# Kernel optimization log

Hardware: AMD Instinct MI355X
Metric: run time of the kernel (lower is better)

Reference implementation:

```python
import jax, jax.numpy as jnp
import numpy as np

MODEL_DIM = 2048
NUM_HEADS = 32
NUM_KV_HEADS = 8
HEAD_DIM = MODEL_DIM // NUM_HEADS  # 64
NUM_REP = NUM_HEADS // NUM_KV_HEADS  # 4


def setup_inputs() -> dict:
    key = jax.random.key(0)
    ks = jax.random.split(key, 6)
    B, S = 1, 2048
    s = 1.0 / np.sqrt(MODEL_DIM)
    x = jax.random.normal(ks[0], (B, S, MODEL_DIM), dtype=jnp.float32)
    # causal mask, 1 = keep, 0 = mask (scores.masked_fill(mask == 0, -1e9))
    mask = jnp.tril(jnp.ones((S, S), dtype=jnp.int32))[None, None, :, :]
    w_q = jax.random.normal(ks[1], (MODEL_DIM, MODEL_DIM), dtype=jnp.float32) * s
    w_k = jax.random.normal(ks[2], (NUM_KV_HEADS * HEAD_DIM, MODEL_DIM), dtype=jnp.float32) * s
    w_v = jax.random.normal(ks[3], (NUM_KV_HEADS * HEAD_DIM, MODEL_DIM), dtype=jnp.float32) * s
    w_o = jax.random.normal(ks[4], (MODEL_DIM, MODEL_DIM), dtype=jnp.float32) * s
    b_o = jax.random.normal(ks[5], (MODEL_DIM,), dtype=jnp.float32) * 0.01
    return {"x": x, "mask": mask, "w_q": w_q, "w_k": w_k, "w_v": w_v, "w_o": w_o, "b_o": b_o}


def reference(x, mask, w_q, w_k, w_v, w_o, b_o):
    B, S, _ = x.shape
    # projections (torch Linear: x @ W.T)
    q = (x @ w_q.T).reshape(B, S, NUM_HEADS, HEAD_DIM).transpose(0, 2, 1, 3)      # [B,H,S,D]
    k = (x @ w_k.T).reshape(B, S, NUM_KV_HEADS, HEAD_DIM).transpose(0, 2, 1, 3)   # [B,Hk,S,D]
    v = (x @ w_v.T).reshape(B, S, NUM_KV_HEADS, HEAD_DIM).transpose(0, 2, 1, 3)   # [B,Hk,S,D]
    # group Q heads by their shared KV head instead of materializing repeated KV
    qg = q.reshape(B, NUM_KV_HEADS, NUM_REP, S, HEAD_DIM)                         # [B,Hk,R,S,D]
    scale = 1.0 / np.sqrt(HEAD_DIM).astype(np.float32)
    scores = jnp.einsum('bgrsd,bgtd->bgrst', qg, k) * scale                       # [B,Hk,R,S,S]
    scores = jnp.where(mask[:, :, None, :, :] == 0, jnp.float32(-1e9), scores)
    attn = jax.nn.softmax(scores, axis=-1)
    ctx = jnp.einsum('bgrst,bgtd->bgrsd', attn, v)                                # [B,Hk,R,S,D]
    ctx = ctx.reshape(B, NUM_HEADS, S, HEAD_DIM).transpose(0, 2, 1, 3).reshape(B, S, MODEL_DIM)
    return ctx @ w_o.T + b_o
```

## Files before the change

### kernel.cpp

```cpp
#include <hip/hip_runtime.h>
#include <hip/hip_bf16.h>

typedef __hip_bfloat16 bf16;
typedef __attribute__((ext_vector_type(8))) short short8;
typedef __attribute__((ext_vector_type(4))) short short4_t;
typedef __attribute__((ext_vector_type(4))) float f32x4;

#define S_LEN 2048
#define DMODEL 2048
#define NH 32
#define NKV 8
#define DH 64

__device__ __forceinline__ int detect_isbf(const void* src) {
    unsigned int wsamp = ((const unsigned int*)src)[(threadIdx.x & 63) * 37];
    int e0 = (wsamp >> 7) & 0xFF;
    unsigned long long mb = __ballot(e0 >= 100 && e0 <= 140);
    return (__popcll(mb) >= 48) ? 1 : 0;
}

__global__ void detect_kernel(const unsigned int* __restrict__ x, int* __restrict__ flag) {
    int tid = threadIdx.x;
    unsigned int w = x[tid * 37];
    int e0 = (w >> 7) & 0xFF;
    int in = (e0 >= 100 && e0 <= 140) ? 1 : 0;
    unsigned long long m = __ballot(in);
    if (tid == 0) flag[0] = (__popcll(m) >= 48) ? 1 : 0;
}

__device__ __forceinline__ void conv8(const void* src, bf16* dst, int i, float scale, int isbf) {
    short8 out;
    if (isbf) {
        short8 v = *(const short8*)((const bf16*)src + i);
        if (scale != 1.0f) {
            #pragma unroll
            for (int j = 0; j < 8; ++j) {
                float f = __bfloat162float(((const bf16*)&v)[j]) * scale;
                ((bf16*)&out)[j] = __float2bfloat16(f);
            }
        } else out = v;
    } else {
        const float* gp = (const float*)src + i;
        f32x4 a = *(const f32x4*)gp;
        f32x4 b = *(const f32x4*)(gp + 4);
        #pragma unroll
        for (int j = 0; j < 4; ++j) ((bf16*)&out)[j]     = __float2bfloat16(a[j] * scale);
        #pragma unroll
        for (int j = 0; j < 4; ++j) ((bf16*)&out)[j + 4] = __float2bfloat16(b[j] * scale);
    }
    *(short8*)(dst + i) = out;
}

__global__ __launch_bounds__(256)
void convert4_kernel(const void* __restrict__ x, const void* __restrict__ wq,
                     const void* __restrict__ wk, const void* __restrict__ wv,
                     bf16* __restrict__ xb, bf16* __restrict__ wqkv) {
    const int b = blockIdx.x;
    const void* src; bf16* dst; int boff; float scale = 1.0f;
    if (b < 2048)       { src = x;  dst = xb;              boff = b;        }
    else if (b < 4096)  { src = wq; dst = wqkv;            boff = b - 2048; scale = 0.125f; }
    else if (b < 4608)  { src = wk; dst = wqkv + 4194304;  boff = b - 4096; }
    else                { src = wv; dst = wqkv + 5242880;  boff = b - 4608; }
    const int isbf = detect_isbf(src);
    int i = (boff * 256 + threadIdx.x) * 8;
    conv8(src, dst, i, scale, isbf);
}

__device__ __forceinline__ void gload_lds16(const void* g, void* l) {
    __builtin_amdgcn_global_load_lds(
        (const __attribute__((address_space(1))) void*)(unsigned long long)(size_t)g,
        (__attribute__((address_space(3))) void*)(unsigned int)(size_t)l,
        16, 0, 0);
}

__device__ __forceinline__ void gemm_core_2ph(const bf16* __restrict__ A, const bf16* __restrict__ B,
                                              int K, int m0, int n0,
                                              bf16* sA, bf16* sB, f32x4 acc[4][2]) {
    const int tid = threadIdx.x;
    const int w = tid >> 6, lane = tid & 63;
    const int wm = (w >> 1) * 64, wn = (w & 1) * 32;
    const int lm = lane & 15, lq = lane >> 4;
    const int xr = lm & 7;

    size_t aoff[4], boff[2];
    #pragma unroll
    for (int r = 0; r < 4; ++r) {
        int ci = w * 256 + r * 64 + lane;
        int row = ci >> 3, c = (ci & 7) ^ (row & 7);
        aoff[r] = (size_t)(m0 + row) * K + c * 8;
    }
    #pragma unroll
    for (int r = 0; r < 2; ++r) {
        int cj = w * 128 + r * 64 + lane;
        int row = cj >> 3, c = (cj & 7) ^ (row & 7);
        boff[r] = (size_t)(n0 + row) * K + c * 8;
    }

    const int nt = K >> 6;
    int cur = 0;

    {
        bf16* la = sA + w * 2048;
        bf16* lb = sB + w * 1024;
        #pragma unroll
        for (int r = 0; r < 4; ++r) gload_lds16(A + aoff[r], la + r * 512);
        #pragma unroll
        for (int r = 0; r < 2; ++r) gload_lds16(B + boff[r], lb + r * 512);
    }
    __syncthreads();

    for (int t = 0; t < nt; ++t) {
        bf16* curA = sA + cur * 8192;
        bf16* curB = sB + cur * 4096;
        if (t + 1 < nt) {
            const int nxt = cur ^ 1;
            const int k0 = (t + 1) << 6;
            bf16* la = sA + nxt * 8192 + w * 2048;
            bf16* lb = sB + nxt * 4096 + w * 1024;
            #pragma unroll
            for (int r = 0; r < 4; ++r) gload_lds16(A + aoff[r] + k0, la + r * 512);
            #pragma unroll
            for (int r = 0; r < 2; ++r) gload_lds16(B + boff[r] + k0, lb + r * 512);
        }

        short8 aF[2][4], bF[2][2];
        #pragma unroll
        for (int ks = 0; ks < 2; ++ks) {
            const int cc = ((ks * 4 + lq) ^ xr) * 8;
            #pragma unroll
            for (int i = 0; i < 4; ++i)
                aF[ks][i] = *(const short8*)&curA[(wm + i * 16 + lm) * 64 + cc];
            #pragma unroll
            for (int j = 0; j < 2; ++j)
                bF[ks][j] = *(const short8*)&curB[(wn + j * 16 + lm) * 64 + cc];
        }

        __builtin_amdgcn_s_setprio(1);
        #pragma unroll
        for (int ks = 0; ks < 2; ++ks)
            #pragma unroll
            for (int i = 0; i < 4; ++i)
                #pragma unroll
                for (int j = 0; j < 2; ++j)
                    acc[i][j] = __builtin_amdgcn_mfma_f32_16x16x32_bf16(aF[ks][i], bF[ks][j], acc[i][j], 0, 0, 0);
        __builtin_amdgcn_s_setprio(0);

        __syncthreads();
        cur ^= 1;
    }
}

template<bool BIAS, bool BIAS_DYN, bool OUT_DYN>
__global__ __launch_bounds__(256, 3)
void gemm_bf16s(const bf16* __restrict__ A, const bf16* __restrict__ B,
                const void* __restrict__ bias, void* __restrict__ C,
                int M, int N, int K, int ldc, const void* __restrict__ xsrc) {
    __shared__ bf16 sA[2 * 128 * 64];
    __shared__ bf16 sB[2 * 64 * 64];
    const int isbf = (BIAS_DYN || OUT_DYN) ? detect_isbf(xsrc) : 1;
    const int tid = threadIdx.x;
    const int m0 = blockIdx.y * 128, n0 = blockIdx.x * 64;
    const int w = tid >> 6, lane = tid & 63;
    const int wm = (w >> 1) * 64, wn = (w & 1) * 32;
    const int lm = lane & 15, lq = lane >> 4;

    f32x4 acc[4][2];
    const f32x4 zero = {0.f, 0.f, 0.f, 0.f};
    for (int i = 0; i < 4; ++i)
        for (int j = 0; j < 2; ++j) acc[i][j] = zero;

    gemm_core_2ph(A, B, K, m0, n0, sA, sB, acc);

    for (int i = 0; i < 4; ++i)
        for (int j = 0; j < 2; ++j)
            for (int r = 0; r < 4; ++r) {
                int row = m0 + wm + i * 16 + lq * 4 + r;
                int col = n0 + wn + j * 16 + lm;
                float v = acc[i][j][r];
                if (BIAS) {
                    if (BIAS_DYN && !isbf) v += ((const float*)bias)[col];
                    else                   v += __bfloat162float(((const bf16*)bias)[col]);
                }
                size_t idx = (size_t)row * ldc + col;
                if (OUT_DYN && !isbf) ((float*)C)[idx] = v;
                else                  ((bf16*)C)[idx] = __float2bfloat16(v);
            }
}

__global__ __launch_bounds__(256, 3)
void gemm_qkv(const bf16* __restrict__ A, const bf16* __restrict__ B,
              bf16* __restrict__ Qo, bf16* __restrict__ Ko, bf16* __restrict__ Vto) {
    __shared__ bf16 sA[2 * 128 * 64];
    __shared__ bf16 sB[2 * 64 * 64];
    const int tid = threadIdx.x;
    const int m0 = blockIdx.y * 128, n0 = blockIdx.x * 64;
    const int w = tid >> 6, lane = tid & 63;
    const int wm = (w >> 1) * 64, wn = (w & 1) * 32;
    const int lm = lane & 15, lq = lane >> 4;

    f32x4 acc[4][2];
    const f32x4 zero = {0.f, 0.f, 0.f, 0.f};
    for (int i = 0; i < 4; ++i)
        for (int j = 0; j < 2; ++j) acc[i][j] = zero;

    gemm_core_2ph(A, B, DMODEL, m0, n0, sA, sB, acc);

    const int route = (n0 < 2048) ? 0 : ((n0 < 2560) ? 1 : 2);
    for (int i = 0; i < 4; ++i)
        for (int j = 0; j < 2; ++j)
            for (int r = 0; r < 4; ++r) {
                int row = m0 + wm + i * 16 + lq * 4 + r;
                int col = n0 + wn + j * 16 + lm;
                bf16 v = __float2bfloat16(acc[i][j][r]);
                if (route == 0)      Qo[(size_t)row * DMODEL + col] = v;
                else if (route == 1) Ko[(size_t)row * (NKV * DH) + (col - 2048)] = v;
                else                 Vto[(size_t)(col - 2560) * S_LEN + row] = v;
            }
}

template<bool TRANS_OUT, bool BIAS, bool A_DYN, bool B_DYN, bool BIAS_DYN, bool OUT_DYN>
__global__ __launch_bounds__(256, 2)
void gemm_bt(const void* __restrict__ A, const void* __restrict__ B,
             const void* __restrict__ bias, void* __restrict__ C,
             int M, int N, int K, int ldc, const int* __restrict__ flagp) {
    __shared__ bf16 sA[128 * 32];
    __shared__ bf16 sB[128 * 32];

    const int isbf = flagp[0];
    const int tid = threadIdx.x;
    const int m0 = blockIdx.y * 128, n0 = blockIdx.x * 128;
    const int w = tid >> 6, lane = tid & 63;
    const int wm = (w >> 1) * 64, wn = (w & 1) * 64;
    const int lm = lane & 15, lq = lane >> 4;

    f32x4 acc[4][4];
    const f32x4 zero = {0.f, 0.f, 0.f, 0.f};
    for (int i = 0; i < 4; ++i)
        for (int j = 0; j < 4; ++j) acc[i][j] = zero;

    for (int k0 = 0; k0 < K; k0 += 32) {
        __syncthreads();
        for (int it = 0; it < 2; ++it) {
            int c = it * 256 + tid;
            int row = c >> 2, off = (c & 3) * 8;
            if (!A_DYN || isbf) {
                *(short8*)&sA[row * 32 + off] =
                    *(const short8*)((const bf16*)A + (size_t)(m0 + row) * K + k0 + off);
            } else {
                const float* gp = (const float*)A + (size_t)(m0 + row) * K + k0 + off;
                #pragma unroll
                for (int i = 0; i < 8; ++i) sA[row * 32 + off + i] = __float2bfloat16(gp[i]);
            }
            if (!B_DYN || isbf) {
                *(short8*)&sB[row * 32 + off] =
                    *(const short8*)((const bf16*)B + (size_t)(n0 + row) * K + k0 + off);
            } else {
                const float* gp = (const float*)B + (size_t)(n0 + row) * K + k0 + off;
                #pragma unroll
                for (int i = 0; i < 8; ++i) sB[row * 32 + off + i] = __float2bfloat16(gp[i]);
            }
        }
        __syncthreads();

        short8 aF[4], bF[4];
        for (int i = 0; i < 4; ++i)
            aF[i] = *(const short8*)&sA[(wm + i * 16 + lm) * 32 + lq * 8];
        for (int i = 0; i < 4; ++i)
            bF[i] = *(const short8*)&sB[(wn + i * 16 + lm) * 32 + lq * 8];
        for (int i = 0; i < 4; ++i)
            for (int j = 0; j < 4; ++j)
                acc[i][j] = __builtin_amdgcn_mfma_f32_16x16x32_bf16(aF[i], bF[j], acc[i][j], 0, 0, 0);
    }

    for (int i = 0; i < 4; ++i)
        for (int j = 0; j < 4; ++j)
            for (int r = 0; r < 4; ++r) {
                int row = m0 + wm + i * 16 + lq * 4 + r;
                int col = n0 + wn + j * 16 + lm;
                float v = acc[i][j][r];
                if (BIAS) {
                    if (BIAS_DYN && !isbf) v += ((const float*)bias)[col];
                    else                   v += __bfloat162float(((const bf16*)bias)[col]);
                }
                size_t idx = TRANS_OUT ? (size_t)col * ldc + row : (size_t)row * ldc + col;
                if (OUT_DYN && !isbf) ((float*)C)[idx] = v;
                else                  ((bf16*)C)[idx] = __float2bfloat16(v);
            }
}

template<bool PRESCALED>
__global__ __launch_bounds__(256, 3)
void attn_kernel(const bf16* __restrict__ Q, const bf16* __restrict__ Km,
                 const bf16* __restrict__ Vt, bf16* __restrict__ ctx,
                 const void* __restrict__ wo_src, bf16* __restrict__ wob) {
    if (blockIdx.y == 32) {
        if (wo_src) {
            const int isbf = detect_isbf(wo_src);
            int i = (blockIdx.x * 256 + threadIdx.x) * 8;
            for (; i < DMODEL * DMODEL; i += 16 * 256 * 8)
                conv8(wo_src, wob, i, 1.0f, isbf);
        }
        return;
    }

    __shared__ bf16 sK[2][64 * 64];
    __shared__ bf16 sV[2][64 * 64];
    __shared__ bf16 sP[4][16 * 72];

    const int tid = threadIdx.x;
    const int h  = blockIdx.y;
    const int kvh = h >> 2;
    const int w = tid >> 6, lane = tid & 63;
    const int lm = lane & 15, lq = lane >> 4;
    const int qloc = w * 16 + lm;
    const int xr = lm & 7;

    int srt[2]; int scs[2];
    #pragma unroll
    for (int i = 0; i < 2; ++i) {
        srt[i] = w * 16 + i * 8 + (lane >> 3);
        scs[i] = (lane & 7) ^ (srt[i] & 7);
    }

    const f32x4 zero = {0.f, 0.f, 0.f, 0.f};

    for (int ph = 0; ph < 2; ++ph) {
        const int qb = ph ? (31 - blockIdx.x) : blockIdx.x;
        const int nt = qb + 1;

        const int qrow = qb * 64 + w * 16 + lm;
        short8 aq0 = *(const short8*)&Q[(size_t)qrow * DMODEL + h * 64 + lq * 8];
        short8 aq1 = *(const short8*)&Q[(size_t)qrow * DMODEL + h * 64 + 32 + lq * 8];

        float m_r = -1e30f, l_r = 0.f;
        f32x4 oacc[4];
        #pragma unroll
        for (int ni = 0; ni < 4; ++ni) oacc[ni] = zero;

        {
            bf16* dk = &sK[0][(w * 16) * 64];
            bf16* dv = &sV[0][(w * 16) * 64];
            #pragma unroll
            for (int i = 0; i < 2; ++i) {
                gload_lds16(&Km[(size_t)srt[i] * (NKV * DH) + kvh * 64 + scs[i] * 8], dk + i * 512);
                gload_lds16(&Vt[(size_t)(kvh * 64 + srt[i]) * S_LEN + scs[i] * 8],    dv + i * 512);
            }
        }
        __syncthreads();

        int cur = 0;
        for (int kt = 0; kt < nt; ++kt) {
            if (kt + 1 < nt) {
                const int b0 = (kt + 1) * 64;
                bf16* dk = &sK[cur ^ 1][(w * 16) * 64];
                bf16* dv = &sV[cur ^ 1][(w * 16) * 64];
                #pragma unroll
                for (int i = 0; i < 2; ++i) {
                    gload_lds16(&Km[(size_t)(b0 + srt[i]) * (NKV * DH) + kvh * 64 + scs[i] * 8], dk + i * 512);
                    gload_lds16(&Vt[(size_t)(kvh * 64 + srt[i]) * S_LEN + b0 + scs[i] * 8],      dv + i * 512);
                }
            }

            f32x4 sacc[4];
            #pragma unroll
            for (int ni = 0; ni < 4; ++ni) sacc[ni] = zero;
            __builtin_amdgcn_s_setprio(1);
            #pragma unroll
            for (int ks = 0; ks < 2; ++ks) {
                short8 aq = ks ? aq1 : aq0;
                #pragma unroll
                for (int ni = 0; ni < 4; ++ni) {
                    short8 bk = *(const short8*)&sK[cur][(ni * 16 + lm) * 64 + ((ks * 4 + lq) ^ xr) * 8];
                    sacc[ni] = __builtin_amdgcn_mfma_f32_16x16x32_bf16(bk, aq, sacc[ni], 0, 0, 0);
                }
            }
            __builtin_amdgcn_s_setprio(0);

            float mx = -3e38f;
            if (kt == nt - 1) {
                #pragma unroll
                for (int ni = 0; ni < 4; ++ni)
                    #pragma unroll
                    for (int r = 0; r < 4; ++r) {
                        float s = sacc[ni][r];
                        if (!PRESCALED) s *= 0.125f;
                        if ((ni * 16 + lq * 4 + r) > qloc) s = -1e30f;
                        sacc[ni][r] = s;
                        mx = fmaxf(mx, s);
                    }
            } else {
                #pragma unroll
                for (int ni = 0; ni < 4; ++ni)
                    #pragma unroll
                    for (int r = 0; r < 4; ++r) {
                        float s = sacc[ni][r];
                        if (!PRESCALED) s *= 0.125f;
                        sacc[ni][r] = s;
                        mx = fmaxf(mx, s);
                    }
            }
            mx = fmaxf(mx, __shfl_xor(mx, 16));
            mx = fmaxf(mx, __shfl_xor(mx, 32));

            int defer = (mx - m_r <= 8.0f) ? 1 : 0;
            if (!__all(defer)) {
                float m_new = fmaxf(m_r, mx);
                float alpha = __expf(m_r - m_new);
                m_r = m_new;
                l_r *= alpha;
                #pragma unroll
                for (int r = 0; r < 4; ++r) {
                    float a_b = __shfl(alpha, (lane & 48) | (lq * 4 + r));
                    #pragma unroll
                    for (int ni = 0; ni < 4; ++ni) oacc[ni][r] *= a_b;
                }
            }

            float rs = 0.f;
            #pragma unroll
            for (int ni = 0; ni < 4; ++ni) {
                short4_t pk;
                #pragma unroll
                for (int r = 0; r < 4; ++r) {
                    float p = __expf(sacc[ni][r] - m_r);
                    rs += p;
                    ((bf16*)&pk)[r] = __float2bfloat16(p);
                }
                *(short4_t*)&sP[w][lm * 72 + ni * 16 + lq * 4] = pk;
            }
            rs += __shfl_xor(rs, 16);
            rs += __shfl_xor(rs, 32);
            l_r += rs;

            asm volatile("s_waitcnt lgkmcnt(0)" ::: "memory");
            __builtin_amdgcn_sched_barrier(0);

            __builtin_amdgcn_s_setprio(1);
            #pragma unroll
            for (int ks = 0; ks < 2; ++ks) {
                short8 ap = *(const short8*)&sP[w][lm * 72 + ks * 32 + lq * 8];
                #pragma unroll
                for (int ni = 0; ni < 4; ++ni) {
                    short8 bv = *(const short8*)&sV[cur][(ni * 16 + lm) * 64 + ((ks * 4 + lq) ^ xr) * 8];
                    oacc[ni] = __builtin_amdgcn_mfma_f32_16x16x32_bf16(ap, bv, oacc[ni], 0, 0, 0);
                }
            }
            __builtin_amdgcn_s_setprio(0);

            __syncthreads();
            cur ^= 1;
        }

        #pragma unroll
        for (int r = 0; r < 4; ++r) {
            float l_b = __shfl(l_r, (lane & 48) | (lq * 4 + r));
            float inv = 1.0f / l_b;
            #pragma unroll
            for (int ni = 0; ni < 4; ++ni)
                ctx[(size_t)(qb * 64 + w * 16 + lq * 4 + r) * DMODEL + h * 64 + ni * 16 + lm] =
                    __float2bfloat16(oacc[ni][r] * inv);
        }
    }
}

extern "C" void kernel_launch(void* const* d_in, const int* in_sizes, int n_in,
                              void* d_out, int out_size, void* d_ws, size_t ws_size,
                              hipStream_t stream) {
    const void* x   = d_in[0];
    const void* w_q = d_in[2];
    const void* w_k = d_in[3];
    const void* w_v = d_in[4];
    const void* w_o = d_in[5];
    const void* b_o = d_in[6];

    const size_t MB = 1024u * 1024u;
    char* ws = (char*)d_ws;
    int*  flag = (int*)ws;
    dim3 blk(256);

    if (ws_size >= 32 * MB + 4096) {
        bf16* xb   = (bf16*)(ws + 4096);
        bf16* wqkv = (bf16*)(ws + 4096 + 8 * MB);
        bf16* Qws  = (bf16*)(ws + 4096 + 20 * MB);
        bf16* Kws  = (bf16*)(ws + 4096 + 28 * MB);
        bf16* Vtws = (bf16*)(ws + 4096 + 30 * MB);
        bf16* wob  = xb;
        bf16* Ctx  = wqkv;

        convert4_kernel<<<5120, blk, 0, stream>>>(x, w_q, w_k, w_v, xb, wqkv);
        gemm_qkv<<<dim3(48, 16), blk, 0, stream>>>(xb, wqkv, Qws, Kws, Vtws);
        attn_kernel<true><<<dim3(16, 33), blk, 0, stream>>>(Qws, Kws, Vtws, Ctx, w_o, wob);
        gemm_bf16s<true, true, true><<<dim3(32, 16), blk, 0, stream>>>(
            Ctx, wob, b_o, d_out, S_LEN, DMODEL, DMODEL, DMODEL, x);
    } else {
        bf16* Qws  = (bf16*)(ws + 4096);
        bf16* Kws  = (bf16*)(ws + 4096 + 8u * MB);
        bf16* Vtws = (bf16*)(ws + 4096 + 10u * MB);
        bf16* Ctx  = (bf16*)(ws + 4096 + 12u * MB);

        detect_kernel<<<1, 64, 0, stream>>>((const unsigned int*)x, flag);
        gemm_bt<false, false, true, true, false, false><<<dim3(16, 16), blk, 0, stream>>>(
            x, w_q, nullptr, Qws, S_LEN, DMODEL, DMODEL, DMODEL, flag);
        gemm_bt<false, false, true, true, false, false><<<dim3(4, 16), blk, 0, stream>>>(
            x, w_k, nullptr, Kws, S_LEN, NKV * DH, DMODEL, NKV * DH, flag);
        gemm_bt<true, false, true, true, false, false><<<dim3(4, 16), blk, 0, stream>>>(
            x, w_v, nullptr, Vtws, S_LEN, NKV * DH, DMODEL, S_LEN, flag);
        attn_kernel<false><<<dim3(16, 32), blk, 0, stream>>>(Qws, Kws, Vtws, Ctx, nullptr, nullptr);
        gemm_bt<false, true, false, true, true, true><<<dim3(16, 16), blk, 0, stream>>>(
            Ctx, w_o, b_o, d_out, S_LEN, DMODEL, DMODEL, DMODEL, flag);
    }
}
```

Before: 238.1 us.

## Process two query heads per attention block to share K/V tiles

Each attention block now runs 512 threads covering two query heads that share one KV head. The K/V tiles are loaded into LDS once and reused by both heads, with half the waves staging K and half staging V. The intent is to halve K/V global traffic and LDS fill work per head. In exchange, block count drops to 256 attention blocks plus 128 w_o conversion blocks, and occupancy is limited to 2 blocks per CU, which could reduce latency hiding.

```diff
diff --git a/kernel.cpp b/kernel.cpp
--- a/kernel.cpp
+++ b/kernel.cpp
@@ -289,15 +289,16 @@
 }
 
 template<bool PRESCALED>
-__global__ __launch_bounds__(256, 3)
+__global__ __launch_bounds__(512, 2)
 void attn_kernel(const bf16* __restrict__ Q, const bf16* __restrict__ Km,
                  const bf16* __restrict__ Vt, bf16* __restrict__ ctx,
                  const void* __restrict__ wo_src, bf16* __restrict__ wob) {
-    if (blockIdx.y == 32) {
+    if (blockIdx.y >= 16) {
         if (wo_src) {
+            const int cb = (blockIdx.y - 16) * 16 + blockIdx.x;
             const int isbf = detect_isbf(wo_src);
-            int i = (blockIdx.x * 256 + threadIdx.x) * 8;
-            for (; i < DMODEL * DMODEL; i += 16 * 256 * 8)
+            int i = (cb * 512 + threadIdx.x) * 8;
+            for (; i < DMODEL * DMODEL; i += 128 * 512 * 8)
                 conv8(wo_src, wob, i, 1.0f, isbf);
         }
         return;
@@ -305,20 +306,25 @@
 
     __shared__ bf16 sK[2][64 * 64];
     __shared__ bf16 sV[2][64 * 64];
-    __shared__ bf16 sP[4][16 * 72];
+    __shared__ bf16 sP[8][16 * 72];
 
     const int tid = threadIdx.x;
-    const int h  = blockIdx.y;
-    const int kvh = h >> 2;
-    const int w = tid >> 6, lane = tid & 63;
+    const int hp = blockIdx.y;
+    const int kvh = hp >> 1;
+    const int w = tid >> 6;
+    const int hw = hp * 2 + (w >> 2);
+    const int wq = w & 3;
+    const int lane = tid & 63;
     const int lm = lane & 15, lq = lane >> 4;
-    const int qloc = w * 16 + lm;
+    const int qloc = wq * 16 + lm;
     const int xr = lm & 7;
 
-    int srt[2]; int scs[2];
+    const bool stageK = (w < 4);
+    const int swv = w & 3;
+    int srt[2], scs[2];
     #pragma unroll
     for (int i = 0; i < 2; ++i) {
-        srt[i] = w * 16 + i * 8 + (lane >> 3);
+        srt[i] = swv * 16 + i * 8 + (lane >> 3);
         scs[i] = (lane & 7) ^ (srt[i] & 7);
     }
 
@@ -328,23 +334,25 @@
         const int qb = ph ? (31 - blockIdx.x) : blockIdx.x;
         const int nt = qb + 1;
 
-        const int qrow = qb * 64 + w * 16 + lm;
-        short8 aq0 = *(const short8*)&Q[(size_t)qrow * DMODEL + h * 64 + lq * 8];
-        short8 aq1 = *(const short8*)&Q[(size_t)qrow * DMODEL + h * 64 + 32 + lq * 8];
+        const int qrow = qb * 64 + qloc;
+        short8 aq0 = *(const short8*)&Q[(size_t)qrow * DMODEL + hw * 64 + lq * 8];
+        short8 aq1 = *(const short8*)&Q[(size_t)qrow * DMODEL + hw * 64 + 32 + lq * 8];
 
         float m_r = -1e30f, l_r = 0.f;
         f32x4 oacc[4];
         #pragma unroll
         for (int ni = 0; ni < 4; ++ni) oacc[ni] = zero;
 
-        {
-            bf16* dk = &sK[0][(w * 16) * 64];
-            bf16* dv = &sV[0][(w * 16) * 64];
-            #pragma unroll
-            for (int i = 0; i < 2; ++i) {
+        if (stageK) {
+            bf16* dk = &sK[0][(swv * 16) * 64];
+            #pragma unroll
+            for (int i = 0; i < 2; ++i)
                 gload_lds16(&Km[(size_t)srt[i] * (NKV * DH) + kvh * 64 + scs[i] * 8], dk + i * 512);
-                gload_lds16(&Vt[(size_t)(kvh * 64 + srt[i]) * S_LEN + scs[i] * 8],    dv + i * 512);
-            }
+        } else {
+            bf16* dv = &sV[0][(swv * 16) * 64];
+            #pragma unroll
+            for (int i = 0; i < 2; ++i)
+                gload_lds16(&Vt[(size_t)(kvh * 64 + srt[i]) * S_LEN + scs[i] * 8], dv + i * 512);
         }
         __syncthreads();
 
@@ -352,12 +360,16 @@
         for (int kt = 0; kt < nt; ++kt) {
             if (kt + 1 < nt) {
                 const int b0 = (kt + 1) * 64;
-                bf16* dk = &sK[cur ^ 1][(w * 16) * 64];
-                bf16* dv = &sV[cur ^ 1][(w * 16) * 64];
-                #pragma unroll
-                for (int i = 0; i < 2; ++i) {
-                    gload_lds16(&Km[(size_t)(b0 + srt[i]) * (NKV * DH) + kvh * 64 + scs[i] * 8], dk + i * 512);
-                    gload_lds16(&Vt[(size_t)(kvh * 64 + srt[i]) * S_LEN + b0 + scs[i] * 8],      dv + i * 512);
+                if (stageK) {
+                    bf16* dk = &sK[cur ^ 1][(swv * 16) * 64];
+                    #pragma unroll
+                    for (int i = 0; i < 2; ++i)
+                        gload_lds16(&Km[(size_t)(b0 + srt[i]) * (NKV * DH) + kvh * 64 + scs[i] * 8], dk + i * 512);
+                } else {
+                    bf16* dv = &sV[cur ^ 1][(swv * 16) * 64];
+                    #pragma unroll
+                    for (int i = 0; i < 2; ++i)
+                        gload_lds16(&Vt[(size_t)(kvh * 64 + srt[i]) * S_LEN + b0 + scs[i] * 8], dv + i * 512);
                 }
             }
 
@@ -457,7 +469,7 @@
             float inv = 1.0f / l_b;
             #pragma unroll
             for (int ni = 0; ni < 4; ++ni)
-                ctx[(size_t)(qb * 64 + w * 16 + lq * 4 + r) * DMODEL + h * 64 + ni * 16 + lm] =
+                ctx[(size_t)(qb * 64 + wq * 16 + lq * 4 + r) * DMODEL + hw * 64 + ni * 16 + lm] =
                     __float2bfloat16(oacc[ni][r] * inv);
         }
     }
@@ -489,7 +501,7 @@
 
         convert4_kernel<<<5120, blk, 0, stream>>>(x, w_q, w_k, w_v, xb, wqkv);
         gemm_qkv<<<dim3(48, 16), blk, 0, stream>>>(xb, wqkv, Qws, Kws, Vtws);
-        attn_kernel<true><<<dim3(16, 33), blk, 0, stream>>>(Qws, Kws, Vtws, Ctx, w_o, wob);
+        attn_kernel<true><<<dim3(16, 24), dim3(512), 0, stream>>>(Qws, Kws, Vtws, Ctx, w_o, wob);
         gemm_bf16s<true, true, true><<<dim3(32, 16), blk, 0, stream>>>(
             Ctx, wob, b_o, d_out, S_LEN, DMODEL, DMODEL, DMODEL, x);
     } else {
@@ -505,7 +517,7 @@
             x, w_k, nullptr, Kws, S_LEN, NKV * DH, DMODEL, NKV * DH, flag);
         gemm_bt<true, false, true, true, false, false><<<dim3(4, 16), blk, 0, stream>>>(
             x, w_v, nullptr, Vtws, S_LEN, NKV * DH, DMODEL, S_LEN, flag);
-        attn_kernel<false><<<dim3(16, 32), blk, 0, stream>>>(Qws, Kws, Vtws, Ctx, nullptr, nullptr);
+        attn_kernel<false><<<dim3(16, 16), dim3(512), 0, stream>>>(Qws, Kws, Vtws, Ctx, nullptr, nullptr);
         gemm_bt<false, true, false, true, true, true><<<dim3(16, 16), blk, 0, stream>>>(
             Ctx, w_o, b_o, d_out, S_LEN, DMODEL, DMODEL, DMODEL, flag);
     }
```

New measurement: 212.7 us. 10.7% less time.
